# Kernel optimization log

Hardware: AMD Instinct MI355X
Metric: run time of the kernel (lower is better)

The kernel has to match this reference:

```python
import jax, jax.numpy as jnp
import numpy as np

S = 2048       # seq_len
D = 1024       # d_model
H = 16         # heads
DK = 64        # d_k = d_v = D // H


def setup_inputs() -> dict:
    key = jax.random.key(0)
    ks = jax.random.split(key, 12)
    sc_in = 1.0 / np.sqrt(D)
    return {
        "Q": jax.random.normal(ks[0], (S, D), jnp.float32),
        "K": jax.random.normal(ks[1], (S, D), jnp.float32),
        "V": jax.random.normal(ks[2], (S, D), jnp.float32),
        # stacked per-head projection weights (torch Linear math: x @ W + b, W stored [in,out])
        "Wq": jax.random.normal(ks[3], (H, D, DK), jnp.float32) * sc_in,
        "bq": jnp.zeros((H, DK), jnp.float32),
        "Wk": jax.random.normal(ks[4], (H, D, DK), jnp.float32) * sc_in,
        "bk": jnp.zeros((H, DK), jnp.float32),
        "Wv": jax.random.normal(ks[5], (H, D, DK), jnp.float32) * sc_in,
        "bv": jnp.zeros((H, DK), jnp.float32),
        "Wo": jax.random.normal(ks[6], (H * DK, D), jnp.float32) * (1.0 / np.sqrt(H * DK)),
        "bo": jnp.zeros((D,), jnp.float32),
    }


def reference(Q, K, V, Wq, bq, Wk, bk, Wv, bv, Wo, bo):
    # per-head projections, all heads at once: [S,D] x [H,D,DK] -> [H,S,DK]
    q = jnp.einsum("sd,hdk->hsk", Q, Wq) + bq[:, None, :]
    k = jnp.einsum("sd,hdk->hsk", K, Wk) + bk[:, None, :]
    v = jnp.einsum("sd,hdk->hsk", V, Wv) + bv[:, None, :]
    # scaled dot-product attention per head: [H,S,S]
    scores = jnp.einsum("hsk,htk->hst", q, k) / jnp.sqrt(jnp.asarray(DK, q.dtype))
    attn = jax.nn.softmax(scores, axis=-1)
    heads = jnp.einsum("hst,htv->hsv", attn, v)          # [H,S,DK]
    concat = heads.transpose(1, 0, 2).reshape(S, H * DK)  # [S, H*DK]
    return concat @ Wo + bo                               # [S, D]
```

## Files before the change

### kernel.cpp

```cpp
#include <hip/hip_runtime.h>
#include <stdint.h>

#define S_LEN 2048
#define D_MODEL 1024
#define NH 16
#define DKV 64

typedef unsigned short u16;
typedef __bf16 bf16x8 __attribute__((ext_vector_type(8)));
typedef float f32x4 __attribute__((ext_vector_type(4)));

__device__ __forceinline__ u16 f2bf(float f) {
  union { float f; uint32_t u; } v; v.f = f;
  uint32_t r = v.u + 0x7FFFu + ((v.u >> 16) & 1u);
  return (u16)(r >> 16);
}
__device__ __forceinline__ uint32_t pkbf(float lo, float hi) {
  union { float f; uint32_t u; } a, b; a.f = lo; b.f = hi;
  return ((b.u + 0x8000u) & 0xFFFF0000u) | ((a.u + 0x8000u) >> 16);
}
__device__ __forceinline__ void gl16(const u16* g, u16* l) {
  __builtin_amdgcn_global_load_lds(
      (const __attribute__((address_space(1))) unsigned int*)g,
      (__attribute__((address_space(3))) unsigned int*)l, 16, 0, 0);
}

__global__ __launch_bounds__(256) void prep_k(
    const float* __restrict__ Q, const float* __restrict__ K,
    const float* __restrict__ V, const float* __restrict__ Wq,
    const float* __restrict__ Wk, const float* __restrict__ Wv,
    const float* __restrict__ Wo, u16* __restrict__ QKVb,
    u16* __restrict__ Wqt, u16* __restrict__ Wkt, u16* __restrict__ Wvt,
    u16* __restrict__ Wot) {
  __shared__ float tile[32][33];
  const int idx = blockIdx.x;
  if (idx < 6144) {
    const int z = idx >> 11, blk = idx & 2047;
    const float* src = (z == 0) ? Q : (z == 1) ? K : V;
    u16* dst = QKVb + (size_t)z * S_LEN * D_MODEL;
    size_t i = ((size_t)blk * 256 + threadIdx.x) * 4;
    const float4 v = *(const float4*)(src + i);
    union { u16 h[4]; uint2 u2; } o;
    o.h[0] = f2bf(v.x); o.h[1] = f2bf(v.y); o.h[2] = f2bf(v.z); o.h[3] = f2bf(v.w);
    *(uint2*)(dst + i) = o.u2;
    return;
  }
  const float* ip; u16* op; int R, C, r0, c0;
  if (idx < 9216) {
    int t = idx - 6144;
    int which = t >> 10, head = (t & 1023) >> 6, tl = t & 63;
    ip = ((which == 0) ? Wq : (which == 1) ? Wk : Wv) + (size_t)head * D_MODEL * DKV;
    op = ((which == 0) ? Wqt : (which == 1) ? Wkt : Wvt) + (size_t)head * D_MODEL * DKV;
    R = D_MODEL; C = DKV; c0 = (tl & 1) * 32; r0 = (tl >> 1) * 32;
  } else {
    int t = idx - 9216;
    ip = Wo; op = Wot; R = D_MODEL; C = D_MODEL;
    c0 = (t & 31) * 32; r0 = (t >> 5) * 32;
  }
  int tr = threadIdx.x >> 5, tc = threadIdx.x & 31;
#pragma unroll
  for (int i = 0; i < 4; i++)
    tile[tr + i * 8][tc] = ip[(size_t)(r0 + tr + i * 8) * C + c0 + tc];
  __syncthreads();
#pragma unroll
  for (int i = 0; i < 4; i++) {
    int c = tr + i * 8;
    op[(size_t)(c0 + c) * R + r0 + tc] = f2bf(tile[tc][c]);
  }
}

__global__ __launch_bounds__(256, 2) void proj_gemm_k(
    const u16* __restrict__ qkvb, const u16* __restrict__ Wqt,
    const u16* __restrict__ Wkt, const u16* __restrict__ Wvt,
    const float* __restrict__ bq, const float* __restrict__ bk,
    const float* __restrict__ bv,
    u16* __restrict__ qb, u16* __restrict__ kb, u16* __restrict__ vT) {
  const int bid = blockIdx.x;
  const int l = (bid & 7) * 96 + (bid >> 3);
  const int z = l >> 8, rem = l & 255;
  const int m0 = (rem >> 4) * 128, n0 = (rem & 15) * 64;
  const u16* A = qkvb + (size_t)z * S_LEN * D_MODEL;
  const u16* Bt = (z == 0) ? Wqt : (z == 1) ? Wkt : Wvt;
  const float* bias = (z == 0) ? bq : (z == 1) ? bk : bv;
  const float scale = (z == 0) ? 0.18033688f : 1.0f;

  __shared__ __align__(16) u16 smem[36864];
  const int tid = threadIdx.x;
  const int w = tid >> 6, lane = tid & 63, quad = lane >> 4, l15 = lane & 15;
  const int wm = (w >> 1) * 64, wn = (w & 1) * 32;
  const int pbA = w * 256, pbB = w * 128;

  f32x4 acc[4][2] = {};

  {
#pragma unroll
    for (int b = 0; b < 2; b++) {
      const int k0 = b * 64;
      u16* As = smem + b * 8192;
      u16* Bs = smem + 24576 + b * 4096;
#pragma unroll
      for (int e = 0; e < 4; e++) {
        int p = pbA + e * 64 + lane;
        int r = p >> 3, cg = (p & 7) ^ (r & 7);
        gl16(&A[(size_t)(m0 + r) * D_MODEL + k0 + cg * 8], As + (pbA + e * 64) * 8);
      }
#pragma unroll
      for (int e = 0; e < 2; e++) {
        int p = pbB + e * 64 + lane;
        int r = p >> 3, cg = (p & 7) ^ (r & 7);
        gl16(&Bt[(size_t)(n0 + r) * D_MODEL + k0 + cg * 8], Bs + (pbB + e * 64) * 8);
      }
    }
  }
#pragma unroll
  for (int it = 0; it < 16; it++) {
    const int rd = it % 3;
    if (it < 15) asm volatile("s_waitcnt vmcnt(6)" ::: "memory");
    else         asm volatile("s_waitcnt vmcnt(0)" ::: "memory");
    __builtin_amdgcn_s_barrier();
    __builtin_amdgcn_sched_barrier(0);
    if (it < 14) {
      const int wr = (rd + 2) % 3;
      const int k0 = (it + 2) * 64;
      u16* As = smem + wr * 8192;
      u16* Bs = smem + 24576 + wr * 4096;
#pragma unroll
      for (int e = 0; e < 4; e++) {
        int p = pbA + e * 64 + lane;
        int r = p >> 3, cg = (p & 7) ^ (r & 7);
        gl16(&A[(size_t)(m0 + r) * D_MODEL + k0 + cg * 8], As + (pbA + e * 64) * 8);
      }
#pragma unroll
      for (int e = 0; e < 2; e++) {
        int p = pbB + e * 64 + lane;
        int r = p >> 3, cg = (p & 7) ^ (r & 7);
        gl16(&Bt[(size_t)(n0 + r) * D_MODEL + k0 + cg * 8], Bs + (pbB + e * 64) * 8);
      }
    }
    const u16* As = smem + rd * 8192;
    const u16* Bs = smem + 24576 + rd * 4096;
#pragma unroll
    for (int kc = 0; kc < 2; kc++) {
      bf16x8 af[4], bfr[2];
      const int c = kc * 4 + quad;
#pragma unroll
      for (int t = 0; t < 4; t++) {
        int ma = wm + t * 16 + l15;
        af[t] = *(const bf16x8*)&As[(ma * 8 + (c ^ (ma & 7))) * 8];
      }
#pragma unroll
      for (int t = 0; t < 2; t++) {
        int na = wn + t * 16 + l15;
        bfr[t] = *(const bf16x8*)&Bs[(na * 8 + (c ^ (na & 7))) * 8];
      }
      __builtin_amdgcn_s_setprio(1);
#pragma unroll
      for (int tm = 0; tm < 4; tm++)
#pragma unroll
        for (int tn = 0; tn < 2; tn++)
          acc[tm][tn] = __builtin_amdgcn_mfma_f32_16x16x32_bf16(af[tm], bfr[tn], acc[tm][tn], 0, 0, 0);
      __builtin_amdgcn_s_setprio(0);
    }
  }

  if (z < 2) {
    u16* O = (z == 0) ? qb : kb;
#pragma unroll
    for (int tm = 0; tm < 4; tm++)
#pragma unroll
      for (int tn = 0; tn < 2; tn++)
#pragma unroll
        for (int r = 0; r < 4; r++) {
          int row = m0 + wm + tm * 16 + quad * 4 + r;
          int col = n0 + wn + tn * 16 + l15;
          O[(size_t)row * D_MODEL + col] = f2bf((acc[tm][tn][r] + bias[col]) * scale);
        }
  } else {
#pragma unroll
    for (int tm = 0; tm < 4; tm++)
#pragma unroll
      for (int tn = 0; tn < 2; tn++) {
        int col = n0 + wn + tn * 16 + l15;
        int row0 = m0 + wm + tm * 16 + quad * 4;
        float b = bias[col];
        union { u16 h[4]; uint2 u2; } o;
#pragma unroll
        for (int r = 0; r < 4; r++) o.h[r] = f2bf(acc[tm][tn][r] + b);
        *(uint2*)&vT[(size_t)col * S_LEN + row0] = o.u2;
      }
  }
}

__global__ __launch_bounds__(512) void attn_k(
    const u16* __restrict__ qb, const u16* __restrict__ kb,
    const u16* __restrict__ vT, u16* __restrict__ conc) {
  const int bid = blockIdx.x;
  const int l = (bid & 7) * 32 + (bid >> 3);
  const int h = l >> 4, qblk = (l & 15) * 128;
  const int tid = threadIdx.x;
  const int w = tid >> 6, lane = tid & 63, quad = lane >> 4, l15 = lane & 15;
  const int half = w >> 2, qg = w & 3;
  const int q0 = qblk + qg * 32;

  __shared__ __align__(16) u16 smem[47104];
  u16* Kh = smem + half * 8192;
  u16* Vh = smem + 16384 + half * 8192;
  u16* Pw = smem + 32768 + w * 1792;

  bf16x8 qf[2][2];
#pragma unroll
  for (int qi = 0; qi < 2; qi++)
#pragma unroll
    for (int kc = 0; kc < 2; kc++)
      qf[qi][kc] = *(const bf16x8*)&qb[(size_t)(q0 + qi * 16 + l15) * D_MODEL + h * 64 + kc * 32 + quad * 8];

  const u16* kbase = kb + (size_t)h * 64;
  const u16* vbase = vT + (size_t)(h * 64) * S_LEN;

  const int p = qg * 64 + lane;
  const int kr = p >> 3, kcg = (p & 7) ^ (kr & 7);
  const int vr = p >> 2, vcg = (p & 3) ^ (vr & 3);
  const size_t kgoff = (size_t)kr * D_MODEL + kcg * 8;
  const size_t vgoff = (size_t)vr * S_LEN + vcg * 8;
  const int ldsoff = qg * 512;

  f32x4 oacc[2][4] = {};
  float lsum0 = 0.f, lsum1 = 0.f;

  {
#pragma unroll
    for (int s = 0; s < 3; s++) {
      const int t0 = half * 1024 + s * 32;
      gl16(kbase + (size_t)t0 * D_MODEL + kgoff, Kh + s * 2048 + ldsoff);
      gl16(vbase + t0 + vgoff, Vh + s * 2048 + ldsoff);
    }
  }

#pragma unroll
  for (int it = 0; it < 32; it++) {
    const int rd = it & 3;
    if (it < 30)       asm volatile("s_waitcnt vmcnt(4)" ::: "memory");
    else if (it == 30) asm volatile("s_waitcnt vmcnt(2)" ::: "memory");
    else               asm volatile("s_waitcnt vmcnt(0)" ::: "memory");
    __builtin_amdgcn_s_barrier();
    __builtin_amdgcn_sched_barrier(0);
    if (it < 29) {
      const int wr = (it + 3) & 3;
      const int t0n = half * 1024 + (it + 3) * 32;
      gl16(kbase + (size_t)t0n * D_MODEL + kgoff, Kh + wr * 2048 + ldsoff);
      gl16(vbase + t0n + vgoff, Vh + wr * 2048 + ldsoff);
    }
    const u16* Kc = Kh + rd * 2048;
    const u16* Vc = Vh + rd * 2048;

    f32x4 sacc[2][2] = {};
    __builtin_amdgcn_s_setprio(1);
#pragma unroll
    for (int kc = 0; kc < 2; kc++)
#pragma unroll
      for (int tn = 0; tn < 2; tn++) {
        int rr = tn * 16 + l15;
        bf16x8 ka = *(const bf16x8*)&Kc[(rr * 8 + ((kc * 4 + quad) ^ (rr & 7))) * 8];
        sacc[0][tn] = __builtin_amdgcn_mfma_f32_16x16x32_bf16(ka, qf[0][kc], sacc[0][tn], 0, 0, 0);
        sacc[1][tn] = __builtin_amdgcn_mfma_f32_16x16x32_bf16(ka, qf[1][kc], sacc[1][tn], 0, 0, 0);
      }
    __builtin_amdgcn_s_setprio(0);

#pragma unroll
    for (int qi = 0; qi < 2; qi++)
#pragma unroll
      for (int tn = 0; tn < 2; tn++) {
        float p0 = __builtin_amdgcn_exp2f(sacc[qi][tn][0]);
        float p1 = __builtin_amdgcn_exp2f(sacc[qi][tn][1]);
        float p2 = __builtin_amdgcn_exp2f(sacc[qi][tn][2]);
        float p3 = __builtin_amdgcn_exp2f(sacc[qi][tn][3]);
        if (qi == 0) lsum0 += (p0 + p1) + (p2 + p3);
        else         lsum1 += (p0 + p1) + (p2 + p3);
        uint2 pw2; pw2.x = pkbf(p0, p1); pw2.y = pkbf(p2, p3);
        *(uint2*)&Pw[(qi * 16 + l15) * 56 + tn * 16 + quad * 4] = pw2;
      }

    bf16x8 pa0 = *(const bf16x8*)&Pw[(l15) * 56 + quad * 8];
    bf16x8 pa1 = *(const bf16x8*)&Pw[(16 + l15) * 56 + quad * 8];
    __builtin_amdgcn_s_setprio(1);
#pragma unroll
    for (int nt = 0; nt < 4; nt++) {
      int dv = nt * 16 + l15;
      bf16x8 vb = *(const bf16x8*)&Vc[(dv * 4 + (quad ^ (dv & 3))) * 8];
      oacc[0][nt] = __builtin_amdgcn_mfma_f32_16x16x32_bf16(pa0, vb, oacc[0][nt], 0, 0, 0);
      oacc[1][nt] = __builtin_amdgcn_mfma_f32_16x16x32_bf16(pa1, vb, oacc[1][nt], 0, 0, 0);
    }
    __builtin_amdgcn_s_setprio(0);
  }
  __syncthreads();

  lsum0 += __shfl_xor(lsum0, 16, 64); lsum0 += __shfl_xor(lsum0, 32, 64);
  lsum1 += __shfl_xor(lsum1, 16, 64); lsum1 += __shfl_xor(lsum1, 32, 64);

  float* OshF = (float*)smem;
  float* lshF = OshF + 8 * 2 * 16 * 68;
  if (lane < 16) {
    lshF[w * 32 + lane] = lsum0;
    lshF[w * 32 + 16 + lane] = lsum1;
  }
#pragma unroll
  for (int qi = 0; qi < 2; qi++)
#pragma unroll
    for (int nt = 0; nt < 4; nt++)
#pragma unroll
      for (int r = 0; r < 4; r++)
        OshF[(w * 2 + qi) * 1088 + (quad * 4 + r) * 68 + nt * 16 + l15] = oacc[qi][nt][r];
  __syncthreads();

  const int q = tid >> 2;
  const int dv0 = (tid & 3) * 16;
  const int qg2 = q >> 5, qi = (q >> 4) & 1, qr = q & 15;
  const float* pa = &OshF[(qg2 * 2 + qi) * 1088 + qr * 68 + dv0];
  const float* pb = &OshF[((qg2 + 4) * 2 + qi) * 1088 + qr * 68 + dv0];
  float4 a0 = *(const float4*)pa, a1 = *(const float4*)(pa + 4);
  float4 a2 = *(const float4*)(pa + 8), a3 = *(const float4*)(pa + 12);
  float4 b0 = *(const float4*)pb, b1 = *(const float4*)(pb + 4);
  float4 b2 = *(const float4*)(pb + 8), b3 = *(const float4*)(pb + 12);
  float li = 1.0f / (lshF[qg2 * 32 + qi * 16 + qr] + lshF[(qg2 + 4) * 32 + qi * 16 + qr]);
  union { u16 hh[8]; uint4 u4; } o0, o1;
  o0.hh[0] = f2bf((a0.x + b0.x) * li); o0.hh[1] = f2bf((a0.y + b0.y) * li);
  o0.hh[2] = f2bf((a0.z + b0.z) * li); o0.hh[3] = f2bf((a0.w + b0.w) * li);
  o0.hh[4] = f2bf((a1.x + b1.x) * li); o0.hh[5] = f2bf((a1.y + b1.y) * li);
  o0.hh[6] = f2bf((a1.z + b1.z) * li); o0.hh[7] = f2bf((a1.w + b1.w) * li);
  o1.hh[0] = f2bf((a2.x + b2.x) * li); o1.hh[1] = f2bf((a2.y + b2.y) * li);
  o1.hh[2] = f2bf((a2.z + b2.z) * li); o1.hh[3] = f2bf((a2.w + b2.w) * li);
  o1.hh[4] = f2bf((a3.x + b3.x) * li); o1.hh[5] = f2bf((a3.y + b3.y) * li);
  o1.hh[6] = f2bf((a3.z + b3.z) * li); o1.hh[7] = f2bf((a3.w + b3.w) * li);
  u16* orow = conc + (size_t)(qblk + q) * D_MODEL + h * 64 + dv0;
  *(uint4*)orow = o0.u4;
  *(uint4*)(orow + 8) = o1.u4;
}

__global__ __launch_bounds__(256, 2) void out_gemm_k(
    const u16* __restrict__ A, const u16* __restrict__ Bt,
    const float* __restrict__ bias, float* __restrict__ out) {
  const int bid = blockIdx.x;
  const int l = (bid & 7) * 64 + (bid >> 3);
  const int m0 = (l >> 4) * 64, n0 = (l & 15) * 64;
  __shared__ __align__(16) u16 smem[8 * 4096];
  const int tid = threadIdx.x;
  const int w = tid >> 6, lane = tid & 63, quad = lane >> 4, l15 = lane & 15;
  const int wm = (w >> 1) * 32, wn = (w & 1) * 32;
  const int pb = w * 128;

  f32x4 acc[2][2] = {};
  {
#pragma unroll
    for (int s = 0; s < 3; s++) {
      const int k0 = s * 64;
#pragma unroll
      for (int e = 0; e < 2; e++) {
        int p = pb + e * 64 + lane;
        int r = p >> 3, cg = (p & 7) ^ (r & 7);
        gl16(&A[(size_t)(m0 + r) * D_MODEL + k0 + cg * 8], smem + s * 4096 + (pb + e * 64) * 8);
        gl16(&Bt[(size_t)(n0 + r) * D_MODEL + k0 + cg * 8], smem + 16384 + s * 4096 + (pb + e * 64) * 8);
      }
    }
  }
#pragma unroll
  for (int it = 0; it < 16; it++) {
    const int rd = it & 3;
    if (it < 14)       asm volatile("s_waitcnt vmcnt(8)" ::: "memory");
    else if (it == 14) asm volatile("s_waitcnt vmcnt(4)" ::: "memory");
    else               asm volatile("s_waitcnt vmcnt(0)" ::: "memory");
    __builtin_amdgcn_s_barrier();
    __builtin_amdgcn_sched_barrier(0);
    if (it < 13) {
      const int wr = (it + 3) & 3;
      const int k0 = (it + 3) * 64;
      u16* As = smem + wr * 4096;
      u16* Bs = smem + 16384 + wr * 4096;
#pragma unroll
      for (int e = 0; e < 2; e++) {
        int p = pb + e * 64 + lane;
        int r = p >> 3, cg = (p & 7) ^ (r & 7);
        gl16(&A[(size_t)(m0 + r) * D_MODEL + k0 + cg * 8], As + (pb + e * 64) * 8);
        gl16(&Bt[(size_t)(n0 + r) * D_MODEL + k0 + cg * 8], Bs + (pb + e * 64) * 8);
      }
    }
    const u16* As = smem + rd * 4096;
    const u16* Bs = smem + 16384 + rd * 4096;
#pragma unroll
    for (int kc = 0; kc < 2; kc++) {
      const int c = kc * 4 + quad;
      bf16x8 af[2], bfr[2];
#pragma unroll
      for (int t = 0; t < 2; t++) {
        int ma = wm + t * 16 + l15, na = wn + t * 16 + l15;
        af[t] = *(const bf16x8*)&As[(ma * 8 + (c ^ (ma & 7))) * 8];
        bfr[t] = *(const bf16x8*)&Bs[(na * 8 + (c ^ (na & 7))) * 8];
      }
      __builtin_amdgcn_s_setprio(1);
#pragma unroll
      for (int tm = 0; tm < 2; tm++)
#pragma unroll
        for (int tn = 0; tn < 2; tn++)
          acc[tm][tn] = __builtin_amdgcn_mfma_f32_16x16x32_bf16(af[tm], bfr[tn], acc[tm][tn], 0, 0, 0);
      __builtin_amdgcn_s_setprio(0);
    }
  }
#pragma unroll
  for (int tm = 0; tm < 2; tm++)
#pragma unroll
    for (int tn = 0; tn < 2; tn++)
#pragma unroll
      for (int r = 0; r < 4; r++) {
        int row = m0 + wm + tm * 16 + quad * 4 + r;
        int col = n0 + wn + tn * 16 + l15;
        out[(size_t)row * D_MODEL + col] = acc[tm][tn][r] + bias[col];
      }
}

extern "C" void kernel_launch(void* const* d_in, const int* in_sizes, int n_in,
                              void* d_out, int out_size, void* d_ws, size_t ws_size,
                              hipStream_t stream) {
  const float* Q  = (const float*)d_in[0];
  const float* K  = (const float*)d_in[1];
  const float* V  = (const float*)d_in[2];
  const float* Wq = (const float*)d_in[3];
  const float* bq = (const float*)d_in[4];
  const float* Wk = (const float*)d_in[5];
  const float* bk = (const float*)d_in[6];
  const float* Wv = (const float*)d_in[7];
  const float* bv = (const float*)d_in[8];
  const float* Wo = (const float*)d_in[9];
  const float* bo = (const float*)d_in[10];
  float* out = (float*)d_out;

  u16* ws = (u16*)d_ws;
  u16* QKVb = ws;
  u16* Wqt  = QKVb + (size_t)3 * S_LEN * D_MODEL;
  u16* Wkt  = Wqt + (size_t)D_MODEL * D_MODEL;
  u16* Wvt  = Wkt + (size_t)D_MODEL * D_MODEL;
  u16* Wot  = Wvt + (size_t)D_MODEL * D_MODEL;
  u16* qbuf = Wot + (size_t)D_MODEL * D_MODEL;
  u16* kbuf = qbuf + (size_t)S_LEN * D_MODEL;
  u16* vTb  = kbuf + (size_t)S_LEN * D_MODEL;
  u16* conc = vTb + (size_t)S_LEN * D_MODEL;

  prep_k<<<dim3(10240), 256, 0, stream>>>(Q, K, V, Wq, Wk, Wv, Wo,
                                          QKVb, Wqt, Wkt, Wvt, Wot);
  proj_gemm_k<<<dim3(768), 256, 0, stream>>>(
      QKVb, Wqt, Wkt, Wvt, bq, bk, bv, qbuf, kbuf, vTb);
  attn_k<<<dim3(256), 512, 0, stream>>>(qbuf, kbuf, vTb, conc);
  out_gemm_k<<<dim3(512), 256, 0, stream>>>(conc, Wot, bo, out);
}
```

Before: 154.8 us.

## Enlarge output GEMM tile to 128x64 with triple-buffered pipeline

The output projection GEMM now uses 128x64 tiles instead of 64x64, so each wave computes a 64x32 sub-tile with 4x2 MFMA accumulators and 256 blocks are launched instead of 512. The shared-memory ring drops from four stages to three, with a prefetch distance of two and adjusted waitcnt thresholds. The larger tile is meant to reuse each B fragment more and cut global and LDS traffic per FLOP. The cost is fewer blocks, roughly one per CU, which limits latency hiding, plus a shallower prefetch.

```diff
diff --git a/kernel.cpp b/kernel.cpp
--- a/kernel.cpp
+++ b/kernel.cpp
@@ -340,64 +340,81 @@
     const u16* __restrict__ A, const u16* __restrict__ Bt,
     const float* __restrict__ bias, float* __restrict__ out) {
   const int bid = blockIdx.x;
-  const int l = (bid & 7) * 64 + (bid >> 3);
-  const int m0 = (l >> 4) * 64, n0 = (l & 15) * 64;
-  __shared__ __align__(16) u16 smem[8 * 4096];
+  const int l = (bid & 7) * 32 + (bid >> 3);
+  const int m0 = (l >> 4) * 128, n0 = (l & 15) * 64;
+
+  __shared__ __align__(16) u16 smem[36864];
   const int tid = threadIdx.x;
   const int w = tid >> 6, lane = tid & 63, quad = lane >> 4, l15 = lane & 15;
-  const int wm = (w >> 1) * 32, wn = (w & 1) * 32;
-  const int pb = w * 128;
-
-  f32x4 acc[2][2] = {};
+  const int wm = (w >> 1) * 64, wn = (w & 1) * 32;
+  const int pbA = w * 256, pbB = w * 128;
+
+  f32x4 acc[4][2] = {};
+
   {
 #pragma unroll
-    for (int s = 0; s < 3; s++) {
-      const int k0 = s * 64;
+    for (int b = 0; b < 2; b++) {
+      const int k0 = b * 64;
+      u16* As = smem + b * 8192;
+      u16* Bs = smem + 24576 + b * 4096;
+#pragma unroll
+      for (int e = 0; e < 4; e++) {
+        int p = pbA + e * 64 + lane;
+        int r = p >> 3, cg = (p & 7) ^ (r & 7);
+        gl16(&A[(size_t)(m0 + r) * D_MODEL + k0 + cg * 8], As + (pbA + e * 64) * 8);
+      }
 #pragma unroll
       for (int e = 0; e < 2; e++) {
-        int p = pb + e * 64 + lane;
-        int r = p >> 3, cg = (p & 7) ^ (r & 7);
-        gl16(&A[(size_t)(m0 + r) * D_MODEL + k0 + cg * 8], smem + s * 4096 + (pb + e * 64) * 8);
-        gl16(&Bt[(size_t)(n0 + r) * D_MODEL + k0 + cg * 8], smem + 16384 + s * 4096 + (pb + e * 64) * 8);
+        int p = pbB + e * 64 + lane;
+        int r = p >> 3, cg = (p & 7) ^ (r & 7);
+        gl16(&Bt[(size_t)(n0 + r) * D_MODEL + k0 + cg * 8], Bs + (pbB + e * 64) * 8);
       }
     }
   }
 #pragma unroll
   for (int it = 0; it < 16; it++) {
-    const int rd = it & 3;
-    if (it < 14)       asm volatile("s_waitcnt vmcnt(8)" ::: "memory");
-    else if (it == 14) asm volatile("s_waitcnt vmcnt(4)" ::: "memory");
-    else               asm volatile("s_waitcnt vmcnt(0)" ::: "memory");
+    const int rd = it % 3;
+    if (it < 15) asm volatile("s_waitcnt vmcnt(6)" ::: "memory");
+    else         asm volatile("s_waitcnt vmcnt(0)" ::: "memory");
     __builtin_amdgcn_s_barrier();
     __builtin_amdgcn_sched_barrier(0);
-    if (it < 13) {
-      const int wr = (it + 3) & 3;
-      const int k0 = (it + 3) * 64;
-      u16* As = smem + wr * 4096;
-      u16* Bs = smem + 16384 + wr * 4096;
+    if (it < 14) {
+      const int wr = (rd + 2) % 3;
+      const int k0 = (it + 2) * 64;
+      u16* As = smem + wr * 8192;
+      u16* Bs = smem + 24576 + wr * 4096;
+#pragma unroll
+      for (int e = 0; e < 4; e++) {
+        int p = pbA + e * 64 + lane;
+        int r = p >> 3, cg = (p & 7) ^ (r & 7);
+        gl16(&A[(size_t)(m0 + r) * D_MODEL + k0 + cg * 8], As + (pbA + e * 64) * 8);
+      }
 #pragma unroll
       for (int e = 0; e < 2; e++) {
-        int p = pb + e * 64 + lane;
-        int r = p >> 3, cg = (p & 7) ^ (r & 7);
-        gl16(&A[(size_t)(m0 + r) * D_MODEL + k0 + cg * 8], As + (pb + e * 64) * 8);
-        gl16(&Bt[(size_t)(n0 + r) * D_MODEL + k0 + cg * 8], Bs + (pb + e * 64) * 8);
-      }
-    }
-    const u16* As = smem + rd * 4096;
-    const u16* Bs = smem + 16384 + rd * 4096;
+        int p = pbB + e * 64 + lane;
+        int r = p >> 3, cg = (p & 7) ^ (r & 7);
+        gl16(&Bt[(size_t)(n0 + r) * D_MODEL + k0 + cg * 8], Bs + (pbB + e * 64) * 8);
+      }
+    }
+    const u16* As = smem + rd * 8192;
+    const u16* Bs = smem + 24576 + rd * 4096;
 #pragma unroll
     for (int kc = 0; kc < 2; kc++) {
+      bf16x8 af[4], bfr[2];
       const int c = kc * 4 + quad;
-      bf16x8 af[2], bfr[2];
+#pragma unroll
+      for (int t = 0; t < 4; t++) {
+        int ma = wm + t * 16 + l15;
+        af[t] = *(const bf16x8*)&As[(ma * 8 + (c ^ (ma & 7))) * 8];
+      }
 #pragma unroll
       for (int t = 0; t < 2; t++) {
-        int ma = wm + t * 16 + l15, na = wn + t * 16 + l15;
-        af[t] = *(const bf16x8*)&As[(ma * 8 + (c ^ (ma & 7))) * 8];
+        int na = wn + t * 16 + l15;
         bfr[t] = *(const bf16x8*)&Bs[(na * 8 + (c ^ (na & 7))) * 8];
       }
       __builtin_amdgcn_s_setprio(1);
 #pragma unroll
-      for (int tm = 0; tm < 2; tm++)
+      for (int tm = 0; tm < 4; tm++)
 #pragma unroll
         for (int tn = 0; tn < 2; tn++)
           acc[tm][tn] = __builtin_amdgcn_mfma_f32_16x16x32_bf16(af[tm], bfr[tn], acc[tm][tn], 0, 0, 0);
@@ -405,7 +422,7 @@
     }
   }
 #pragma unroll
-  for (int tm = 0; tm < 2; tm++)
+  for (int tm = 0; tm < 4; tm++)
 #pragma unroll
     for (int tn = 0; tn < 2; tn++)
 #pragma unroll
@@ -448,5 +465,5 @@
   proj_gemm_k<<<dim3(768), 256, 0, stream>>>(
       QKVb, Wqt, Wkt, Wvt, bq, bk, bv, qbuf, kbuf, vTb);
   attn_k<<<dim3(256), 512, 0, stream>>>(qbuf, kbuf, vTb, conc);
-  out_gemm_k<<<dim3(512), 256, 0, stream>>>(conc, Wot, bo, out);
-}
+  out_gemm_k<<<dim3(256), 256, 0, stream>>>(conc, Wot, bo, out);
+}
```

After: 156.2 us. About the same (+0.9%).

## Fuse fp32-to-bf16 input conversion into projection GEMM loads

Applied to the files above, without the earlier changes.

Removes the separate pass that converted Q, K and V to bf16 in the prep kernel. The projection GEMM now loads fp32 activations into registers, converts them, and writes bf16 tiles to shared memory. The pipeline goes from a triple-buffered async global-to-LDS scheme to double buffering with register prefetch and a __syncthreads per iteration. This avoids writing and re-reading a 12 MB bf16 intermediate, at the cost of doubled global read width for A, more register pressure, and weaker load/compute overlap.

```diff
diff --git a/kernel.cpp b/kernel.cpp
--- a/kernel.cpp
+++ b/kernel.cpp
@@ -26,34 +26,20 @@
 }
 
 __global__ __launch_bounds__(256) void prep_k(
-    const float* __restrict__ Q, const float* __restrict__ K,
-    const float* __restrict__ V, const float* __restrict__ Wq,
-    const float* __restrict__ Wk, const float* __restrict__ Wv,
-    const float* __restrict__ Wo, u16* __restrict__ QKVb,
+    const float* __restrict__ Wq, const float* __restrict__ Wk,
+    const float* __restrict__ Wv, const float* __restrict__ Wo,
     u16* __restrict__ Wqt, u16* __restrict__ Wkt, u16* __restrict__ Wvt,
     u16* __restrict__ Wot) {
   __shared__ float tile[32][33];
   const int idx = blockIdx.x;
-  if (idx < 6144) {
-    const int z = idx >> 11, blk = idx & 2047;
-    const float* src = (z == 0) ? Q : (z == 1) ? K : V;
-    u16* dst = QKVb + (size_t)z * S_LEN * D_MODEL;
-    size_t i = ((size_t)blk * 256 + threadIdx.x) * 4;
-    const float4 v = *(const float4*)(src + i);
-    union { u16 h[4]; uint2 u2; } o;
-    o.h[0] = f2bf(v.x); o.h[1] = f2bf(v.y); o.h[2] = f2bf(v.z); o.h[3] = f2bf(v.w);
-    *(uint2*)(dst + i) = o.u2;
-    return;
-  }
   const float* ip; u16* op; int R, C, r0, c0;
-  if (idx < 9216) {
-    int t = idx - 6144;
-    int which = t >> 10, head = (t & 1023) >> 6, tl = t & 63;
+  if (idx < 3072) {
+    int which = idx >> 10, head = (idx & 1023) >> 6, tl = idx & 63;
     ip = ((which == 0) ? Wq : (which == 1) ? Wk : Wv) + (size_t)head * D_MODEL * DKV;
     op = ((which == 0) ? Wqt : (which == 1) ? Wkt : Wvt) + (size_t)head * D_MODEL * DKV;
     R = D_MODEL; C = DKV; c0 = (tl & 1) * 32; r0 = (tl >> 1) * 32;
   } else {
-    int t = idx - 9216;
+    int t = idx - 3072;
     ip = Wo; op = Wot; R = D_MODEL; C = D_MODEL;
     c0 = (t & 31) * 32; r0 = (t >> 5) * 32;
   }
@@ -70,7 +56,8 @@
 }
 
 __global__ __launch_bounds__(256, 2) void proj_gemm_k(
-    const u16* __restrict__ qkvb, const u16* __restrict__ Wqt,
+    const float* __restrict__ Qf, const float* __restrict__ Kf,
+    const float* __restrict__ Vf, const u16* __restrict__ Wqt,
     const u16* __restrict__ Wkt, const u16* __restrict__ Wvt,
     const float* __restrict__ bq, const float* __restrict__ bk,
     const float* __restrict__ bv,
@@ -79,66 +66,60 @@
   const int l = (bid & 7) * 96 + (bid >> 3);
   const int z = l >> 8, rem = l & 255;
   const int m0 = (rem >> 4) * 128, n0 = (rem & 15) * 64;
-  const u16* A = qkvb + (size_t)z * S_LEN * D_MODEL;
+  const float* A = (z == 0) ? Qf : (z == 1) ? Kf : Vf;
   const u16* Bt = (z == 0) ? Wqt : (z == 1) ? Wkt : Wvt;
   const float* bias = (z == 0) ? bq : (z == 1) ? bk : bv;
   const float scale = (z == 0) ? 0.18033688f : 1.0f;
 
-  __shared__ __align__(16) u16 smem[36864];
+  __shared__ __align__(16) u16 smem[24576];
   const int tid = threadIdx.x;
   const int w = tid >> 6, lane = tid & 63, quad = lane >> 4, l15 = lane & 15;
   const int wm = (w >> 1) * 64, wn = (w & 1) * 32;
   const int pbA = w * 256, pbB = w * 128;
 
   f32x4 acc[4][2] = {};
+  float4 fa[4][2];
 
   {
 #pragma unroll
-    for (int b = 0; b < 2; b++) {
-      const int k0 = b * 64;
-      u16* As = smem + b * 8192;
-      u16* Bs = smem + 24576 + b * 4096;
+    for (int e = 0; e < 4; e++) {
+      int p = pbA + e * 64 + lane, r = p >> 3, cg = (p & 7) ^ (r & 7);
+      const float* src = &A[(size_t)(m0 + r) * D_MODEL + cg * 8];
+      fa[e][0] = *(const float4*)src;
+      fa[e][1] = *(const float4*)(src + 4);
+    }
+#pragma unroll
+    for (int e = 0; e < 4; e++) {
+      int p = pbA + e * 64 + lane;
+      union { __bf16 b[8]; uint4 u4; } cv;
+      cv.b[0] = (__bf16)fa[e][0].x; cv.b[1] = (__bf16)fa[e][0].y;
+      cv.b[2] = (__bf16)fa[e][0].z; cv.b[3] = (__bf16)fa[e][0].w;
+      cv.b[4] = (__bf16)fa[e][1].x; cv.b[5] = (__bf16)fa[e][1].y;
+      cv.b[6] = (__bf16)fa[e][1].z; cv.b[7] = (__bf16)fa[e][1].w;
+      *(uint4*)&smem[p * 8] = cv.u4;
+    }
+#pragma unroll
+    for (int e = 0; e < 2; e++) {
+      int p = pbB + e * 64 + lane, r = p >> 3, cg = (p & 7) ^ (r & 7);
+      gl16(&Bt[(size_t)(n0 + r) * D_MODEL + cg * 8], smem + 16384 + (pbB + e * 64) * 8);
+    }
+  }
+
+  for (int it = 0; it < 16; it++) {
+    const int cur = it & 1;
+    if (it < 15) {
+      const int k0 = (it + 1) * 64;
 #pragma unroll
       for (int e = 0; e < 4; e++) {
-        int p = pbA + e * 64 + lane;
-        int r = p >> 3, cg = (p & 7) ^ (r & 7);
-        gl16(&A[(size_t)(m0 + r) * D_MODEL + k0 + cg * 8], As + (pbA + e * 64) * 8);
-      }
-#pragma unroll
-      for (int e = 0; e < 2; e++) {
-        int p = pbB + e * 64 + lane;
-        int r = p >> 3, cg = (p & 7) ^ (r & 7);
-        gl16(&Bt[(size_t)(n0 + r) * D_MODEL + k0 + cg * 8], Bs + (pbB + e * 64) * 8);
-      }
-    }
-  }
-#pragma unroll
-  for (int it = 0; it < 16; it++) {
-    const int rd = it % 3;
-    if (it < 15) asm volatile("s_waitcnt vmcnt(6)" ::: "memory");
-    else         asm volatile("s_waitcnt vmcnt(0)" ::: "memory");
-    __builtin_amdgcn_s_barrier();
-    __builtin_amdgcn_sched_barrier(0);
-    if (it < 14) {
-      const int wr = (rd + 2) % 3;
-      const int k0 = (it + 2) * 64;
-      u16* As = smem + wr * 8192;
-      u16* Bs = smem + 24576 + wr * 4096;
-#pragma unroll
-      for (int e = 0; e < 4; e++) {
-        int p = pbA + e * 64 + lane;
-        int r = p >> 3, cg = (p & 7) ^ (r & 7);
-        gl16(&A[(size_t)(m0 + r) * D_MODEL + k0 + cg * 8], As + (pbA + e * 64) * 8);
-      }
-#pragma unroll
-      for (int e = 0; e < 2; e++) {
-        int p = pbB + e * 64 + lane;
-        int r = p >> 3, cg = (p & 7) ^ (r & 7);
-        gl16(&Bt[(size_t)(n0 + r) * D_MODEL + k0 + cg * 8], Bs + (pbB + e * 64) * 8);
-      }
-    }
-    const u16* As = smem + rd * 8192;
-    const u16* Bs = smem + 24576 + rd * 4096;
+        int p = pbA + e * 64 + lane, r = p >> 3, cg = (p & 7) ^ (r & 7);
+        const float* src = &A[(size_t)(m0 + r) * D_MODEL + k0 + cg * 8];
+        fa[e][0] = *(const float4*)src;
+        fa[e][1] = *(const float4*)(src + 4);
+      }
+    }
+    __syncthreads();
+    const u16* As = smem + cur * 8192;
+    const u16* Bs = smem + 16384 + cur * 4096;
 #pragma unroll
     for (int kc = 0; kc < 2; kc++) {
       bf16x8 af[4], bfr[2];
@@ -160,6 +141,26 @@
         for (int tn = 0; tn < 2; tn++)
           acc[tm][tn] = __builtin_amdgcn_mfma_f32_16x16x32_bf16(af[tm], bfr[tn], acc[tm][tn], 0, 0, 0);
       __builtin_amdgcn_s_setprio(0);
+    }
+    if (it < 15) {
+      u16* Aw = smem + (cur ^ 1) * 8192;
+      u16* Bw = smem + 16384 + (cur ^ 1) * 4096;
+#pragma unroll
+      for (int e = 0; e < 4; e++) {
+        int p = pbA + e * 64 + lane;
+        union { __bf16 b[8]; uint4 u4; } cv;
+        cv.b[0] = (__bf16)fa[e][0].x; cv.b[1] = (__bf16)fa[e][0].y;
+        cv.b[2] = (__bf16)fa[e][0].z; cv.b[3] = (__bf16)fa[e][0].w;
+        cv.b[4] = (__bf16)fa[e][1].x; cv.b[5] = (__bf16)fa[e][1].y;
+        cv.b[6] = (__bf16)fa[e][1].z; cv.b[7] = (__bf16)fa[e][1].w;
+        *(uint4*)&Aw[p * 8] = cv.u4;
+      }
+      const int k0 = (it + 1) * 64;
+#pragma unroll
+      for (int e = 0; e < 2; e++) {
+        int p = pbB + e * 64 + lane, r = p >> 3, cg = (p & 7) ^ (r & 7);
+        gl16(&Bt[(size_t)(n0 + r) * D_MODEL + k0 + cg * 8], Bw + (pbB + e * 64) * 8);
+      }
     }
   }
 
@@ -433,8 +434,7 @@
   float* out = (float*)d_out;
 
   u16* ws = (u16*)d_ws;
-  u16* QKVb = ws;
-  u16* Wqt  = QKVb + (size_t)3 * S_LEN * D_MODEL;
+  u16* Wqt  = ws;
   u16* Wkt  = Wqt + (size_t)D_MODEL * D_MODEL;
   u16* Wvt  = Wkt + (size_t)D_MODEL * D_MODEL;
   u16* Wot  = Wvt + (size_t)D_MODEL * D_MODEL;
@@ -443,10 +443,9 @@
   u16* vTb  = kbuf + (size_t)S_LEN * D_MODEL;
   u16* conc = vTb + (size_t)S_LEN * D_MODEL;
 
-  prep_k<<<dim3(10240), 256, 0, stream>>>(Q, K, V, Wq, Wk, Wv, Wo,
-                                          QKVb, Wqt, Wkt, Wvt, Wot);
+  prep_k<<<dim3(4096), 256, 0, stream>>>(Wq, Wk, Wv, Wo, Wqt, Wkt, Wvt, Wot);
   proj_gemm_k<<<dim3(768), 256, 0, stream>>>(
-      QKVb, Wqt, Wkt, Wvt, bq, bk, bv, qbuf, kbuf, vTb);
+      Q, K, V, Wqt, Wkt, Wvt, bq, bk, bv, qbuf, kbuf, vTb);
   attn_k<<<dim3(256), 512, 0, stream>>>(qbuf, kbuf, vTb, conc);
   out_gemm_k<<<dim3(512), 256, 0, stream>>>(conc, Wot, bo, out);
 }
```

Measured after the change: 159.0 us (median of 2 runs). 1.03x slower.
